# Kernel optimization log

Measured on AMD Instinct MI355X. Metric: run time of the kernel, lower is better.

## Reference

```python
import jax, jax.numpy as jnp
import numpy as np
import math

BS, SEQ, DIM, H, LK = 4, 4096, 768, 12, 256
HD = DIM // H  # 64
WIN = SEQ // LK  # 16, AdaptiveAvgPool1d reduces to uniform windows since SEQ % LK == 0


def setup_inputs() -> dict:
    key = jax.random.key(0)
    ks = jax.random.split(key, 12)
    s = 1.0 / math.sqrt(DIM)
    return {
        "query": jax.random.normal(ks[0], (BS, SEQ, DIM), jnp.float32),
        "key": jax.random.normal(ks[1], (BS, SEQ, DIM), jnp.float32),
        "value": jax.random.normal(ks[2], (BS, SEQ, DIM), jnp.float32),
        "mask": jax.random.normal(ks[3], (BS, SEQ), jnp.float32),  # mask<0 -> padded
        "Wq": jax.random.normal(ks[4], (DIM, DIM), jnp.float32) * s,
        "bq": jnp.zeros((DIM,), jnp.float32),
        "Wk": jax.random.normal(ks[5], (DIM, DIM), jnp.float32) * s,
        "bk": jnp.zeros((DIM,), jnp.float32),
        "Wv": jax.random.normal(ks[6], (DIM, DIM), jnp.float32) * s,
        "bv": jnp.zeros((DIM,), jnp.float32),
        "Wo": jax.random.normal(ks[7], (DIM, DIM), jnp.float32) * s,
        "bo": jnp.zeros((DIM,), jnp.float32),
    }


def reference(query, key, value, mask, Wq, bq, Wk, bk, Wv, bv, Wo, bo):
    bs, q_len, _ = query.shape
    # projections (nn.Linear: x @ W.T + b)
    Q = query @ Wq.T + bq
    K = key @ Wk.T + bk
    V = value @ Wv.T + bv
    # mask-fill padded K/V rows with 0 (mask dim==2 path: bool_mask = mask < 0)
    keep = (mask >= 0)[:, :, None]  # [bs, seq, 1]
    K = jnp.where(keep, K, 0.0)
    V = jnp.where(keep, V, 0.0)
    # adaptive avg pool over sequence -> linformer_k=256 (uniform windows of 16)
    Kc = K.reshape(bs, LK, WIN, DIM).mean(axis=2)  # [bs, 256, dim]
    Vc = V.reshape(bs, LK, WIN, DIM).mean(axis=2)
    # split heads
    Qh = Q.reshape(bs, q_len, H, HD) / math.sqrt(HD)  # scale fused
    Kh = Kc.reshape(bs, LK, H, HD)
    Vh = Vc.reshape(bs, LK, H, HD)
    # low-rank attention: [bs, h, q_len, 256]
    scores = jnp.einsum("bqhd,bkhd->bhqk", Qh, Kh)
    weights = jax.nn.softmax(scores, axis=-1)
    context = jnp.einsum("bhqk,bkhd->bqhd", weights, Vh).reshape(bs, q_len, DIM)
    return context @ Wo.T + bo
```

## Files before the change

### kernel.cpp

```cpp
#include <hip/hip_runtime.h>

#define BS_   4
#define SEQ_  4096
#define DIM_  768
#define NH_   12
#define HD_   64
#define LK_   256

typedef __attribute__((ext_vector_type(8))) short          bf8;
typedef __attribute__((ext_vector_type(8))) unsigned short us8;
typedef __attribute__((ext_vector_type(4))) unsigned short us4;
typedef __attribute__((ext_vector_type(4))) float          f32x4;

typedef unsigned int u32g __attribute__((address_space(1)));
typedef unsigned int u32l __attribute__((address_space(3)));

#define LOG2E 1.44269504088896340736f

__device__ __forceinline__ unsigned short f2bf(float f) {
  unsigned u = __builtin_bit_cast(unsigned, f);
  u += 0x7fffu + ((u >> 16) & 1u);
  return (unsigned short)(u >> 16);
}

__device__ __forceinline__ us8 cvt8(const float* __restrict__ p) {
  const float4 a = *(const float4*)p;
  const float4 b = *(const float4*)(p + 4);
  us8 r;
  r[0] = f2bf(a.x); r[1] = f2bf(a.y); r[2] = f2bf(a.z); r[3] = f2bf(a.w);
  r[4] = f2bf(b.x); r[5] = f2bf(b.y); r[6] = f2bf(b.z); r[7] = f2bf(b.w);
  return r;
}

__global__ __launch_bounds__(256) void cvtbf_kernel(
    const float* __restrict__ query,
    const float* __restrict__ Wq, const float* __restrict__ Wk,
    const float* __restrict__ Wv, const float* __restrict__ Wo,
    unsigned short* __restrict__ Qbf, unsigned short* __restrict__ Wbf)
{
  const int i = blockIdx.x * 256 + threadIdx.x;
  const int QN8 = (BS_ * SEQ_ * DIM_) / 8;
  const int WN8 = (DIM_ * DIM_) / 8;
  if (i < QN8) { *(us8*)(Qbf + (size_t)i * 8) = cvt8(query + (size_t)i * 8); return; }
  int j = i - QN8;
  const float* src; unsigned short* dst;
  if      (j <     WN8) { src = Wq; dst = Wbf;                   }
  else if (j < 2 * WN8) { src = Wk; dst = Wbf + DIM_*DIM_;     j -=     WN8; }
  else if (j < 3 * WN8) { src = Wv; dst = Wbf + 2*DIM_*DIM_;   j -= 2 * WN8; }
  else if (j < 4 * WN8) { src = Wo; dst = Wbf + 3*DIM_*DIM_;   j -= 3 * WN8; }
  else return;
  *(us8*)(dst + (size_t)j * 8) = cvt8(src + (size_t)j * 8);
}

__global__ __launch_bounds__(384) void pool_kernel(
    const float* __restrict__ key, const float* __restrict__ value,
    const float* __restrict__ mask,
    unsigned short* __restrict__ pk, unsigned short* __restrict__ pv,
    float* __restrict__ frac)
{
  const int blk = blockIdx.x;
  const int b = blk >> 8;
  const int l = blk & 255;
  const int tid = threadIdx.x;
  __shared__ float keep[16];
  if (tid < 16) keep[tid] = (mask[b * SEQ_ + l * 16 + tid] >= 0.f) ? 1.f : 0.f;
  __syncthreads();
  const int isV = tid >= 192;
  const int c = isV ? tid - 192 : tid;
  const float* src = isV ? value : key;
  float4 acc = make_float4(0.f, 0.f, 0.f, 0.f);
  #pragma unroll 1
  for (int w = 0; w < 16; ++w) {
    if (keep[w] != 0.f) {
      const float4 v = *(const float4*)(src + (size_t)(b * SEQ_ + l * 16 + w) * DIM_ + c * 4);
      acc.x += v.x; acc.y += v.y; acc.z += v.z; acc.w += v.w;
    }
  }
  const float s = 1.f / 16.f;
  unsigned short* dst = isV ? pv : pk;
  us4 o4;
  o4[0] = f2bf(acc.x * s); o4[1] = f2bf(acc.y * s);
  o4[2] = f2bf(acc.z * s); o4[3] = f2bf(acc.w * s);
  *(us4*)(dst + (size_t)(b * LK_ + l) * DIM_ + c * 4) = o4;
  if (tid == 0) {
    float cnt = 0.f;
    for (int w = 0; w < 16; ++w) cnt += keep[w];
    frac[b * LK_ + l] = cnt * s;
  }
}

template<int MODE, int SWZ>
__global__ __launch_bounds__(256) void gemm_bt(
    const void* __restrict__ Aptr_, const void* __restrict__ Bptr_,
    const float* __restrict__ bias, const float* __restrict__ bias2,
    const float* __restrict__ frac,
    void* __restrict__ Cout, float scale)
{
  constexpr int K = DIM_;
  __shared__ __align__(16) unsigned short lA[128 * 32];
  __shared__ __align__(16) unsigned short lB[128 * 32];
  const int tid  = threadIdx.x;
  const int lane = tid & 63;
  const int wave = tid >> 6;

  int bx, by;
  if (SWZ) {
    const int r = (blockIdx.x & 7) * 96 + (blockIdx.x >> 3);
    bx = r / 6; by = r % 6;
  } else {
    bx = blockIdx.x; by = blockIdx.y;
  }
  const int brow = bx * 128;
  const int bcol = by * 128;

  const unsigned short* A = (const unsigned short*)Aptr_;
  const unsigned short* Bw = (const unsigned short*)Bptr_;
  const float* bb = bias;
  int isV = 0;
  if (MODE == 34) {
    isV = blockIdx.z;
    A  += (size_t)isV * (BS_ * LK_ * DIM_);
    Bw += (size_t)isV * (DIM_ * DIM_);
    if (isV) bb = bias2;
  }

  const int wr   = (wave >> 1) * 64;
  const int wc   = (wave & 1) * 64;
  const int fr   = lane & 15;
  const int fk   = (lane >> 4) * 8;

  f32x4 acc[4][4];
  #pragma unroll
  for (int i = 0; i < 4; ++i)
    #pragma unroll
    for (int j = 0; j < 4; ++j) acc[i][j] = (f32x4){0.f, 0.f, 0.f, 0.f};

  const int srow = tid >> 2;
  const int schk = (tid & 3) * 8;

  for (int k0 = 0; k0 < K; k0 += 32) {
    __syncthreads();
    __builtin_amdgcn_global_load_lds(
        (const u32g*)(A + (size_t)(brow + srow) * K + k0 + schk),
        (u32l*)&lA[tid * 8], 16, 0, 0);
    __builtin_amdgcn_global_load_lds(
        (const u32g*)(A + (size_t)(brow + srow + 64) * K + k0 + schk),
        (u32l*)&lA[2048 + tid * 8], 16, 0, 0);
    __builtin_amdgcn_global_load_lds(
        (const u32g*)(Bw + (size_t)(bcol + srow) * K + k0 + schk),
        (u32l*)&lB[tid * 8], 16, 0, 0);
    __builtin_amdgcn_global_load_lds(
        (const u32g*)(Bw + (size_t)(bcol + srow + 64) * K + k0 + schk),
        (u32l*)&lB[2048 + tid * 8], 16, 0, 0);
    __syncthreads();
    bf8 af[4], bfv[4];
    #pragma unroll
    for (int mi = 0; mi < 4; ++mi)
      af[mi] = *(const bf8*)&lA[(wr + mi * 16 + fr) * 32 + fk];
    #pragma unroll
    for (int ni = 0; ni < 4; ++ni)
      bfv[ni] = *(const bf8*)&lB[(wc + ni * 16 + fr) * 32 + fk];
    #pragma unroll
    for (int mi = 0; mi < 4; ++mi)
      #pragma unroll
      for (int ni = 0; ni < 4; ++ni)
        acc[mi][ni] = __builtin_amdgcn_mfma_f32_16x16x32_bf16(af[mi], bfv[ni], acc[mi][ni], 0, 0, 0);
  }

  const int er = (lane >> 4) * 4;
  #pragma unroll
  for (int mi = 0; mi < 4; ++mi) {
    #pragma unroll
    for (int ni = 0; ni < 4; ++ni) {
      #pragma unroll
      for (int j = 0; j < 4; ++j) {
        const int r = brow + wr + mi * 16 + er + j;
        const int c = bcol + wc + ni * 16 + fr;
        float v = acc[mi][ni][j];
        if (MODE == 0) {
          v = (v + bias[c]) * scale;
          ((unsigned short*)Cout)[(size_t)r * DIM_ + c] = f2bf(v);
        } else if (MODE == 2) {
          ((float*)Cout)[(size_t)r * DIM_ + c] = v + bias[c];
        } else {
          v += frac[r] * bb[c];
          const int bb_ = r >> 8, key = r & 255;
          const int hh = c >> 6, dd = c & 63;
          const int bh = bb_ * NH_ + hh;
          size_t idx;
          if (isV) {
            idx = (size_t)bh * 16384 +
                ((key >> 5) * 4 + (dd >> 4)) * 512 + ((key >> 3) & 3) * 128 +
                (dd & 15) * 8 + (key & 7) + 786432;
          } else {
            const int t = key >> 5, g = (key >> 3) & 3, sub = (key >> 2) & 1, jj = key & 3;
            const int frk = g * 4 + jj;
            idx = (size_t)bh * 16384 +
                (((t * 2 + sub) * 2) + (dd >> 5)) * 512 + ((dd >> 3) & 3) * 128 +
                frk * 8 + (dd & 7);
          }
          ((unsigned short*)Cout)[idx] = f2bf(v);
        }
      }
    }
  }
}

__global__ __launch_bounds__(256) void attn_fused(
    const unsigned short* __restrict__ Qh,
    const unsigned short* __restrict__ Kf,
    const unsigned short* __restrict__ Vf,
    unsigned short* __restrict__ ctx)
{
  const int tid  = threadIdx.x;
  const int lane = tid & 63;
  const int wave = tid >> 6;
  const int bh = blockIdx.y;
  const int b = bh / NH_, h = bh % NH_;
  const int fr = lane & 15;
  const int hi = lane >> 4;
  const int qrow = blockIdx.x * 64 + wave * 16;

  const unsigned short* qp = Qh + (size_t)(b * SEQ_ + qrow + fr) * DIM_ + h * HD_ + hi * 8;
  const bf8 q0 = *(const bf8*)qp;
  const bf8 q1 = *(const bf8*)(qp + 32);

  const unsigned short* kb = Kf + (size_t)bh * 16384 + lane * 8;
  f32x4 scA[8], scB[8];
  __builtin_amdgcn_s_setprio(1);
  #pragma unroll
  for (int s = 0; s < 8; ++s) {
    const bf8 ka0 = *(const bf8*)(kb + (s * 4 + 0) * 512);
    const bf8 ka1 = *(const bf8*)(kb + (s * 4 + 1) * 512);
    const bf8 kb0 = *(const bf8*)(kb + (s * 4 + 2) * 512);
    const bf8 kb1 = *(const bf8*)(kb + (s * 4 + 3) * 512);
    f32x4 x = (f32x4){0.f, 0.f, 0.f, 0.f};
    x = __builtin_amdgcn_mfma_f32_16x16x32_bf16(ka0, q0, x, 0, 0, 0);
    x = __builtin_amdgcn_mfma_f32_16x16x32_bf16(ka1, q1, x, 0, 0, 0);
    scA[s] = x;
    f32x4 y = (f32x4){0.f, 0.f, 0.f, 0.f};
    y = __builtin_amdgcn_mfma_f32_16x16x32_bf16(kb0, q0, y, 0, 0, 0);
    y = __builtin_amdgcn_mfma_f32_16x16x32_bf16(kb1, q1, y, 0, 0, 0);
    scB[s] = y;
  }
  __builtin_amdgcn_s_setprio(0);

  float m = -1e30f;
  #pragma unroll
  for (int s = 0; s < 8; ++s)
    #pragma unroll
    for (int j = 0; j < 4; ++j) { m = fmaxf(m, scA[s][j]); m = fmaxf(m, scB[s][j]); }
  m = fmaxf(m, __shfl_xor(m, 16));
  m = fmaxf(m, __shfl_xor(m, 32));
  float sum = 0.f;
  #pragma unroll
  for (int s = 0; s < 8; ++s)
    #pragma unroll
    for (int j = 0; j < 4; ++j) {
      const float pa = exp2f(scA[s][j] - m); scA[s][j] = pa; sum += pa;
      const float pb = exp2f(scB[s][j] - m); scB[s][j] = pb; sum += pb;
    }
  sum += __shfl_xor(sum, 16);
  sum += __shfl_xor(sum, 32);
  const float inv = 1.f / sum;

  bf8 pa[8];
  #pragma unroll
  for (int s = 0; s < 8; ++s) {
    bf8 p;
    #pragma unroll
    for (int j = 0; j < 4; ++j) {
      p[j]     = (short)f2bf(scA[s][j] * inv);
      p[4 + j] = (short)f2bf(scB[s][j] * inv);
    }
    pa[s] = p;
  }

  const unsigned short* vb = Vf + (size_t)bh * 16384 + lane * 8;
  f32x4 acc[4];
  #pragma unroll
  for (int ct = 0; ct < 4; ++ct) acc[ct] = (f32x4){0.f, 0.f, 0.f, 0.f};
  __builtin_amdgcn_s_setprio(1);
  #pragma unroll
  for (int s = 0; s < 8; ++s) {
    #pragma unroll
    for (int ct = 0; ct < 4; ++ct) {
      const bf8 vf = *(const bf8*)(vb + (s * 4 + ct) * 512);
      acc[ct] = __builtin_amdgcn_mfma_f32_16x16x32_bf16(pa[s], vf, acc[ct], 0, 0, 0);
    }
  }
  __builtin_amdgcn_s_setprio(0);

  #pragma unroll
  for (int ct = 0; ct < 4; ++ct)
    #pragma unroll
    for (int j = 0; j < 4; ++j)
      ctx[(size_t)(b * SEQ_ + qrow + hi * 4 + j) * DIM_ + h * HD_ + ct * 16 + fr] =
          f2bf(acc[ct][j]);
}

extern "C" void kernel_launch(void* const* d_in, const int* in_sizes, int n_in,
                              void* d_out, int out_size, void* d_ws, size_t ws_size,
                              hipStream_t stream) {
  const float* query = (const float*)d_in[0];
  const float* key   = (const float*)d_in[1];
  const float* value = (const float*)d_in[2];
  const float* mask  = (const float*)d_in[3];
  const float* Wq    = (const float*)d_in[4];
  const float* bq    = (const float*)d_in[5];
  const float* Wk    = (const float*)d_in[6];
  const float* bk    = (const float*)d_in[7];
  const float* Wv    = (const float*)d_in[8];
  const float* bv    = (const float*)d_in[9];
  const float* Wo    = (const float*)d_in[10];
  const float* bo    = (const float*)d_in[11];
  float* out = (float*)d_out;

  char* ws = (char*)d_ws;
  unsigned short* Qh  = (unsigned short*)ws;
  unsigned short* ctx = (unsigned short*)(ws + 25165824);
  unsigned short* pK  = (unsigned short*)(ws + 50331648);
  unsigned short* pV  = (unsigned short*)(ws + 51904512);
  unsigned short* Kf  = (unsigned short*)(ws + 53477376);
  unsigned short* Vf  = (unsigned short*)(ws + 55050240);
  float*          frac = (float*)(ws + 56623104);
  unsigned short* Wbf = (unsigned short*)(ws + 56627200);
  unsigned short* Qbf = ctx;

  const float qscale = 0.125f * LOG2E;

  pool_kernel<<<dim3(1024), dim3(384), 0, stream>>>(key, value, mask, pK, pV, frac);
  cvtbf_kernel<<<dim3(7296), dim3(256), 0, stream>>>(query, Wq, Wk, Wv, Wo, Qbf, Wbf);
  gemm_bt<0, 1><<<dim3(768), dim3(256), 0, stream>>>(
      Qbf, Wbf, bq, nullptr, nullptr, Qh, qscale);
  gemm_bt<34, 0><<<dim3(8, 6, 2), dim3(256), 0, stream>>>(
      pK, Wbf + DIM_*DIM_, bk, bv, frac, Kf, 1.f);
  attn_fused<<<dim3(64, 48), dim3(256), 0, stream>>>(Qh, Kf, Vf, ctx);
  gemm_bt<2, 1><<<dim3(768), dim3(256), 0, stream>>>(
      ctx, Wbf + 3*DIM_*DIM_, bo, nullptr, nullptr, out, 1.f);
}
```

Measured before the change: 140.3 us.

## Fuse query fp32-to-bf16 conversion into Q GEMM and double attention rows per wave

Drops the separate pass that converts the query tensor to bf16. The Q projection GEMM now loads fp32 query tiles straight from global memory, converts them in registers and writes them to LDS, which saves writing and re-reading a 25MB intermediate. The attention kernel now has each wave process 32 query rows instead of 16, reusing every K/V fragment load for two MFMA chains, with half as many blocks and a launch-bounds occupancy hint. The GEMM A-side loses the async global-to-LDS load path and does synchronous register loads, and the attention kernel uses more registers.

```diff
diff --git a/kernel.cpp b/kernel.cpp
--- a/kernel.cpp
+++ b/kernel.cpp
@@ -33,16 +33,13 @@
 }
 
 __global__ __launch_bounds__(256) void cvtbf_kernel(
-    const float* __restrict__ query,
     const float* __restrict__ Wq, const float* __restrict__ Wk,
     const float* __restrict__ Wv, const float* __restrict__ Wo,
-    unsigned short* __restrict__ Qbf, unsigned short* __restrict__ Wbf)
+    unsigned short* __restrict__ Wbf)
 {
   const int i = blockIdx.x * 256 + threadIdx.x;
-  const int QN8 = (BS_ * SEQ_ * DIM_) / 8;
   const int WN8 = (DIM_ * DIM_) / 8;
-  if (i < QN8) { *(us8*)(Qbf + (size_t)i * 8) = cvt8(query + (size_t)i * 8); return; }
-  int j = i - QN8;
+  int j = i;
   const float* src; unsigned short* dst;
   if      (j <     WN8) { src = Wq; dst = Wbf;                   }
   else if (j < 2 * WN8) { src = Wk; dst = Wbf + DIM_*DIM_;     j -=     WN8; }
@@ -89,7 +86,7 @@
   }
 }
 
-template<int MODE, int SWZ>
+template<int SA, int MODE, int SWZ>
 __global__ __launch_bounds__(256) void gemm_bt(
     const void* __restrict__ Aptr_, const void* __restrict__ Bptr_,
     const float* __restrict__ bias, const float* __restrict__ bias2,
@@ -114,6 +111,7 @@
   const int bcol = by * 128;
 
   const unsigned short* A = (const unsigned short*)Aptr_;
+  const float*          Af = (const float*)Aptr_;
   const unsigned short* Bw = (const unsigned short*)Bptr_;
   const float* bb = bias;
   int isV = 0;
@@ -139,13 +137,23 @@
   const int schk = (tid & 3) * 8;
 
   for (int k0 = 0; k0 < K; k0 += 32) {
+    us8 a0, a1;
+    if (SA == 1) {
+      a0 = cvt8(Af + (size_t)(brow + srow) * K + k0 + schk);
+      a1 = cvt8(Af + (size_t)(brow + srow + 64) * K + k0 + schk);
+    }
     __syncthreads();
-    __builtin_amdgcn_global_load_lds(
-        (const u32g*)(A + (size_t)(brow + srow) * K + k0 + schk),
-        (u32l*)&lA[tid * 8], 16, 0, 0);
-    __builtin_amdgcn_global_load_lds(
-        (const u32g*)(A + (size_t)(brow + srow + 64) * K + k0 + schk),
-        (u32l*)&lA[2048 + tid * 8], 16, 0, 0);
+    if (SA == 0) {
+      __builtin_amdgcn_global_load_lds(
+          (const u32g*)(A + (size_t)(brow + srow) * K + k0 + schk),
+          (u32l*)&lA[tid * 8], 16, 0, 0);
+      __builtin_amdgcn_global_load_lds(
+          (const u32g*)(A + (size_t)(brow + srow + 64) * K + k0 + schk),
+          (u32l*)&lA[2048 + tid * 8], 16, 0, 0);
+    } else {
+      *(us8*)&lA[tid * 8]        = a0;
+      *(us8*)&lA[2048 + tid * 8] = a1;
+    }
     __builtin_amdgcn_global_load_lds(
         (const u32g*)(Bw + (size_t)(bcol + srow) * K + k0 + schk),
         (u32l*)&lB[tid * 8], 16, 0, 0);
@@ -206,7 +214,7 @@
   }
 }
 
-__global__ __launch_bounds__(256) void attn_fused(
+__global__ __launch_bounds__(256, 2) void attn_fused(
     const unsigned short* __restrict__ Qh,
     const unsigned short* __restrict__ Kf,
     const unsigned short* __restrict__ Vf,
@@ -219,14 +227,17 @@
   const int b = bh / NH_, h = bh % NH_;
   const int fr = lane & 15;
   const int hi = lane >> 4;
-  const int qrow = blockIdx.x * 64 + wave * 16;
-
-  const unsigned short* qp = Qh + (size_t)(b * SEQ_ + qrow + fr) * DIM_ + h * HD_ + hi * 8;
-  const bf8 q0 = *(const bf8*)qp;
-  const bf8 q1 = *(const bf8*)(qp + 32);
+  const int qrow0 = blockIdx.x * 128 + wave * 32;
+
+  const unsigned short* qp0 = Qh + (size_t)(b * SEQ_ + qrow0 + fr) * DIM_ + h * HD_ + hi * 8;
+  const unsigned short* qp1 = qp0 + 16 * DIM_;
+  const bf8 q00 = *(const bf8*)qp0;
+  const bf8 q01 = *(const bf8*)(qp0 + 32);
+  const bf8 q10 = *(const bf8*)qp1;
+  const bf8 q11 = *(const bf8*)(qp1 + 32);
 
   const unsigned short* kb = Kf + (size_t)bh * 16384 + lane * 8;
-  f32x4 scA[8], scB[8];
+  f32x4 sA0[8], sB0[8], sA1[8], sB1[8];
   __builtin_amdgcn_s_setprio(1);
   #pragma unroll
   for (int s = 0; s < 8; ++s) {
@@ -234,59 +245,84 @@
     const bf8 ka1 = *(const bf8*)(kb + (s * 4 + 1) * 512);
     const bf8 kb0 = *(const bf8*)(kb + (s * 4 + 2) * 512);
     const bf8 kb1 = *(const bf8*)(kb + (s * 4 + 3) * 512);
-    f32x4 x = (f32x4){0.f, 0.f, 0.f, 0.f};
-    x = __builtin_amdgcn_mfma_f32_16x16x32_bf16(ka0, q0, x, 0, 0, 0);
-    x = __builtin_amdgcn_mfma_f32_16x16x32_bf16(ka1, q1, x, 0, 0, 0);
-    scA[s] = x;
-    f32x4 y = (f32x4){0.f, 0.f, 0.f, 0.f};
-    y = __builtin_amdgcn_mfma_f32_16x16x32_bf16(kb0, q0, y, 0, 0, 0);
-    y = __builtin_amdgcn_mfma_f32_16x16x32_bf16(kb1, q1, y, 0, 0, 0);
-    scB[s] = y;
+    f32x4 x0 = (f32x4){0.f, 0.f, 0.f, 0.f};
+    x0 = __builtin_amdgcn_mfma_f32_16x16x32_bf16(ka0, q00, x0, 0, 0, 0);
+    x0 = __builtin_amdgcn_mfma_f32_16x16x32_bf16(ka1, q01, x0, 0, 0, 0);
+    sA0[s] = x0;
+    f32x4 y0 = (f32x4){0.f, 0.f, 0.f, 0.f};
+    y0 = __builtin_amdgcn_mfma_f32_16x16x32_bf16(kb0, q00, y0, 0, 0, 0);
+    y0 = __builtin_amdgcn_mfma_f32_16x16x32_bf16(kb1, q01, y0, 0, 0, 0);
+    sB0[s] = y0;
+    f32x4 x1 = (f32x4){0.f, 0.f, 0.f, 0.f};
+    x1 = __builtin_amdgcn_mfma_f32_16x16x32_bf16(ka0, q10, x1, 0, 0, 0);
+    x1 = __builtin_amdgcn_mfma_f32_16x16x32_bf16(ka1, q11, x1, 0, 0, 0);
+    sA1[s] = x1;
+    f32x4 y1 = (f32x4){0.f, 0.f, 0.f, 0.f};
+    y1 = __builtin_amdgcn_mfma_f32_16x16x32_bf16(kb0, q10, y1, 0, 0, 0);
+    y1 = __builtin_amdgcn_mfma_f32_16x16x32_bf16(kb1, q11, y1, 0, 0, 0);
+    sB1[s] = y1;
   }
   __builtin_amdgcn_s_setprio(0);
 
-  float m = -1e30f;
+  float m0 = -1e30f, m1 = -1e30f;
   #pragma unroll
   for (int s = 0; s < 8; ++s)
     #pragma unroll
-    for (int j = 0; j < 4; ++j) { m = fmaxf(m, scA[s][j]); m = fmaxf(m, scB[s][j]); }
-  m = fmaxf(m, __shfl_xor(m, 16));
-  m = fmaxf(m, __shfl_xor(m, 32));
-  float sum = 0.f;
+    for (int j = 0; j < 4; ++j) {
+      m0 = fmaxf(m0, sA0[s][j]); m0 = fmaxf(m0, sB0[s][j]);
+      m1 = fmaxf(m1, sA1[s][j]); m1 = fmaxf(m1, sB1[s][j]);
+    }
+  m0 = fmaxf(m0, __shfl_xor(m0, 16));
+  m0 = fmaxf(m0, __shfl_xor(m0, 32));
+  m1 = fmaxf(m1, __shfl_xor(m1, 16));
+  m1 = fmaxf(m1, __shfl_xor(m1, 32));
+  float u0 = 0.f, u1 = 0.f;
   #pragma unroll
   for (int s = 0; s < 8; ++s)
     #pragma unroll
     for (int j = 0; j < 4; ++j) {
-      const float pa = exp2f(scA[s][j] - m); scA[s][j] = pa; sum += pa;
-      const float pb = exp2f(scB[s][j] - m); scB[s][j] = pb; sum += pb;
-    }
-  sum += __shfl_xor(sum, 16);
-  sum += __shfl_xor(sum, 32);
-  const float inv = 1.f / sum;
-
-  bf8 pa[8];
+      float p;
+      p = exp2f(sA0[s][j] - m0); sA0[s][j] = p; u0 += p;
+      p = exp2f(sB0[s][j] - m0); sB0[s][j] = p; u0 += p;
+      p = exp2f(sA1[s][j] - m1); sA1[s][j] = p; u1 += p;
+      p = exp2f(sB1[s][j] - m1); sB1[s][j] = p; u1 += p;
+    }
+  u0 += __shfl_xor(u0, 16);
+  u0 += __shfl_xor(u0, 32);
+  u1 += __shfl_xor(u1, 16);
+  u1 += __shfl_xor(u1, 32);
+  const float inv0 = 1.f / u0;
+  const float inv1 = 1.f / u1;
+
+  bf8 pa0[8], pa1[8];
   #pragma unroll
   for (int s = 0; s < 8; ++s) {
-    bf8 p;
+    bf8 p0, p1;
     #pragma unroll
     for (int j = 0; j < 4; ++j) {
-      p[j]     = (short)f2bf(scA[s][j] * inv);
-      p[4 + j] = (short)f2bf(scB[s][j] * inv);
-    }
-    pa[s] = p;
+      p0[j]     = (short)f2bf(sA0[s][j] * inv0);
+      p0[4 + j] = (short)f2bf(sB0[s][j] * inv0);
+      p1[j]     = (short)f2bf(sA1[s][j] * inv1);
+      p1[4 + j] = (short)f2bf(sB1[s][j] * inv1);
+    }
+    pa0[s] = p0; pa1[s] = p1;
   }
 
   const unsigned short* vb = Vf + (size_t)bh * 16384 + lane * 8;
-  f32x4 acc[4];
-  #pragma unroll
-  for (int ct = 0; ct < 4; ++ct) acc[ct] = (f32x4){0.f, 0.f, 0.f, 0.f};
+  f32x4 acc0[4], acc1[4];
+  #pragma unroll
+  for (int ct = 0; ct < 4; ++ct) {
+    acc0[ct] = (f32x4){0.f, 0.f, 0.f, 0.f};
+    acc1[ct] = (f32x4){0.f, 0.f, 0.f, 0.f};
+  }
   __builtin_amdgcn_s_setprio(1);
   #pragma unroll
   for (int s = 0; s < 8; ++s) {
     #pragma unroll
     for (int ct = 0; ct < 4; ++ct) {
       const bf8 vf = *(const bf8*)(vb + (s * 4 + ct) * 512);
-      acc[ct] = __builtin_amdgcn_mfma_f32_16x16x32_bf16(pa[s], vf, acc[ct], 0, 0, 0);
+      acc0[ct] = __builtin_amdgcn_mfma_f32_16x16x32_bf16(pa0[s], vf, acc0[ct], 0, 0, 0);
+      acc1[ct] = __builtin_amdgcn_mfma_f32_16x16x32_bf16(pa1[s], vf, acc1[ct], 0, 0, 0);
     }
   }
   __builtin_amdgcn_s_setprio(0);
@@ -294,9 +330,12 @@
   #pragma unroll
   for (int ct = 0; ct < 4; ++ct)
     #pragma unroll
-    for (int j = 0; j < 4; ++j)
-      ctx[(size_t)(b * SEQ_ + qrow + hi * 4 + j) * DIM_ + h * HD_ + ct * 16 + fr] =
-          f2bf(acc[ct][j]);
+    for (int j = 0; j < 4; ++j) {
+      ctx[(size_t)(b * SEQ_ + qrow0 + hi * 4 + j) * DIM_ + h * HD_ + ct * 16 + fr] =
+          f2bf(acc0[ct][j]);
+      ctx[(size_t)(b * SEQ_ + qrow0 + 16 + hi * 4 + j) * DIM_ + h * HD_ + ct * 16 + fr] =
+          f2bf(acc1[ct][j]);
+    }
 }
 
 extern "C" void kernel_launch(void* const* d_in, const int* in_sizes, int n_in,
@@ -325,17 +364,16 @@
   unsigned short* Vf  = (unsigned short*)(ws + 55050240);
   float*          frac = (float*)(ws + 56623104);
   unsigned short* Wbf = (unsigned short*)(ws + 56627200);
-  unsigned short* Qbf = ctx;
 
   const float qscale = 0.125f * LOG2E;
 
   pool_kernel<<<dim3(1024), dim3(384), 0, stream>>>(key, value, mask, pK, pV, frac);
-  cvtbf_kernel<<<dim3(7296), dim3(256), 0, stream>>>(query, Wq, Wk, Wv, Wo, Qbf, Wbf);
-  gemm_bt<0, 1><<<dim3(768), dim3(256), 0, stream>>>(
-      Qbf, Wbf, bq, nullptr, nullptr, Qh, qscale);
-  gemm_bt<34, 0><<<dim3(8, 6, 2), dim3(256), 0, stream>>>(
+  cvtbf_kernel<<<dim3(1152), dim3(256), 0, stream>>>(Wq, Wk, Wv, Wo, Wbf);
+  gemm_bt<1, 0, 1><<<dim3(768), dim3(256), 0, stream>>>(
+      query, Wbf, bq, nullptr, nullptr, Qh, qscale);
+  gemm_bt<0, 34, 0><<<dim3(8, 6, 2), dim3(256), 0, stream>>>(
       pK, Wbf + DIM_*DIM_, bk, bv, frac, Kf, 1.f);
-  attn_fused<<<dim3(64, 48), dim3(256), 0, stream>>>(Qh, Kf, Vf, ctx);
-  gemm_bt<2, 1><<<dim3(768), dim3(256), 0, stream>>>(
+  attn_fused<<<dim3(32, 48), dim3(256), 0, stream>>>(Qh, Kf, Vf, ctx);
+  gemm_bt<0, 2, 1><<<dim3(768), dim3(256), 0, stream>>>(
       ctx, Wbf + 3*DIM_*DIM_, bo, nullptr, nullptr, out, 1.f);
 }
```

After: 152.1 us. +8.4%, slower.

## Fuse fp32 query conversion into Q GEMM and merge Q/KV projections into one launch

Applied to the files above, without the earlier changes.

The separate pass that converted the fp32 query to bf16 in a scratch buffer is removed. The Q projection GEMM now loads fp32 query rows into registers, converts them and stores them to LDS, and it shares one launch with the K/V projection blocks, with blocks indexed past 768 handling K/V. The softmax max and sum reductions in attention are restructured into vectorized tree reductions. This avoids a 50MB-scale write and read of the bf16 query copy plus one launch, but the Q path loses the async global-to-LDS load and now stalls on register loads before each LDS store.

```diff
diff --git a/kernel.cpp b/kernel.cpp
--- a/kernel.cpp
+++ b/kernel.cpp
@@ -32,17 +32,21 @@
   return r;
 }
 
+__device__ __forceinline__ f32x4 max4(f32x4 a, f32x4 b) {
+  f32x4 r;
+  r[0] = fmaxf(a[0], b[0]); r[1] = fmaxf(a[1], b[1]);
+  r[2] = fmaxf(a[2], b[2]); r[3] = fmaxf(a[3], b[3]);
+  return r;
+}
+
 __global__ __launch_bounds__(256) void cvtbf_kernel(
-    const float* __restrict__ query,
     const float* __restrict__ Wq, const float* __restrict__ Wk,
     const float* __restrict__ Wv, const float* __restrict__ Wo,
-    unsigned short* __restrict__ Qbf, unsigned short* __restrict__ Wbf)
+    unsigned short* __restrict__ Wbf)
 {
   const int i = blockIdx.x * 256 + threadIdx.x;
-  const int QN8 = (BS_ * SEQ_ * DIM_) / 8;
   const int WN8 = (DIM_ * DIM_) / 8;
-  if (i < QN8) { *(us8*)(Qbf + (size_t)i * 8) = cvt8(query + (size_t)i * 8); return; }
-  int j = i - QN8;
+  int j = i;
   const float* src; unsigned short* dst;
   if      (j <     WN8) { src = Wq; dst = Wbf;                   }
   else if (j < 2 * WN8) { src = Wk; dst = Wbf + DIM_*DIM_;     j -=     WN8; }
@@ -89,12 +93,13 @@
   }
 }
 
-template<int MODE, int SWZ>
-__global__ __launch_bounds__(256) void gemm_bt(
-    const void* __restrict__ Aptr_, const void* __restrict__ Bptr_,
-    const float* __restrict__ bias, const float* __restrict__ bias2,
-    const float* __restrict__ frac,
-    void* __restrict__ Cout, float scale)
+__global__ __launch_bounds__(256) void gemm_qkv(
+    const float* __restrict__ query, const unsigned short* __restrict__ Wbf,
+    const float* __restrict__ bq, const float* __restrict__ bk,
+    const float* __restrict__ bv, const float* __restrict__ frac,
+    const unsigned short* __restrict__ pKV,
+    unsigned short* __restrict__ Qh, unsigned short* __restrict__ KVf,
+    float qscale)
 {
   constexpr int K = DIM_;
   __shared__ __align__(16) unsigned short lA[128 * 32];
@@ -102,32 +107,31 @@
   const int tid  = threadIdx.x;
   const int lane = tid & 63;
   const int wave = tid >> 6;
-
-  int bx, by;
-  if (SWZ) {
-    const int r = (blockIdx.x & 7) * 96 + (blockIdx.x >> 3);
+  const int bid  = blockIdx.x;
+  const int isQ  = bid < 768;
+
+  int bx, by, isV = 0;
+  const unsigned short* Abf = nullptr;
+  const unsigned short* Bw;
+  if (isQ) {
+    const int r = (bid & 7) * 96 + (bid >> 3);
     bx = r / 6; by = r % 6;
+    Bw = Wbf;
   } else {
-    bx = blockIdx.x; by = blockIdx.y;
+    int kid = bid - 768;
+    isV = kid >= 48;
+    kid -= isV * 48;
+    bx = kid / 6; by = kid % 6;
+    Abf = pKV + (size_t)isV * (BS_ * LK_ * DIM_);
+    Bw  = Wbf + (size_t)(1 + isV) * (DIM_ * DIM_);
   }
   const int brow = bx * 128;
   const int bcol = by * 128;
 
-  const unsigned short* A = (const unsigned short*)Aptr_;
-  const unsigned short* Bw = (const unsigned short*)Bptr_;
-  const float* bb = bias;
-  int isV = 0;
-  if (MODE == 34) {
-    isV = blockIdx.z;
-    A  += (size_t)isV * (BS_ * LK_ * DIM_);
-    Bw += (size_t)isV * (DIM_ * DIM_);
-    if (isV) bb = bias2;
-  }
-
-  const int wr   = (wave >> 1) * 64;
-  const int wc   = (wave & 1) * 64;
-  const int fr   = lane & 15;
-  const int fk   = (lane >> 4) * 8;
+  const int wr = (wave >> 1) * 64;
+  const int wc = (wave & 1) * 64;
+  const int fr = lane & 15;
+  const int fk = (lane >> 4) * 8;
 
   f32x4 acc[4][4];
   #pragma unroll
@@ -139,13 +143,23 @@
   const int schk = (tid & 3) * 8;
 
   for (int k0 = 0; k0 < K; k0 += 32) {
+    us8 a0, a1;
+    if (isQ) {
+      a0 = cvt8(query + (size_t)(brow + srow) * K + k0 + schk);
+      a1 = cvt8(query + (size_t)(brow + srow + 64) * K + k0 + schk);
+    }
     __syncthreads();
-    __builtin_amdgcn_global_load_lds(
-        (const u32g*)(A + (size_t)(brow + srow) * K + k0 + schk),
-        (u32l*)&lA[tid * 8], 16, 0, 0);
-    __builtin_amdgcn_global_load_lds(
-        (const u32g*)(A + (size_t)(brow + srow + 64) * K + k0 + schk),
-        (u32l*)&lA[2048 + tid * 8], 16, 0, 0);
+    if (isQ) {
+      *(us8*)&lA[tid * 8]        = a0;
+      *(us8*)&lA[2048 + tid * 8] = a1;
+    } else {
+      __builtin_amdgcn_global_load_lds(
+          (const u32g*)(Abf + (size_t)(brow + srow) * K + k0 + schk),
+          (u32l*)&lA[tid * 8], 16, 0, 0);
+      __builtin_amdgcn_global_load_lds(
+          (const u32g*)(Abf + (size_t)(brow + srow + 64) * K + k0 + schk),
+          (u32l*)&lA[2048 + tid * 8], 16, 0, 0);
+    }
     __builtin_amdgcn_global_load_lds(
         (const u32g*)(Bw + (size_t)(bcol + srow) * K + k0 + schk),
         (u32l*)&lB[tid * 8], 16, 0, 0);
@@ -177,13 +191,11 @@
         const int r = brow + wr + mi * 16 + er + j;
         const int c = bcol + wc + ni * 16 + fr;
         float v = acc[mi][ni][j];
-        if (MODE == 0) {
-          v = (v + bias[c]) * scale;
-          ((unsigned short*)Cout)[(size_t)r * DIM_ + c] = f2bf(v);
-        } else if (MODE == 2) {
-          ((float*)Cout)[(size_t)r * DIM_ + c] = v + bias[c];
+        if (isQ) {
+          v = (v + bq[c]) * qscale;
+          Qh[(size_t)r * DIM_ + c] = f2bf(v);
         } else {
-          v += frac[r] * bb[c];
+          v += frac[r] * (isV ? bv[c] : bk[c]);
           const int bb_ = r >> 8, key = r & 255;
           const int hh = c >> 6, dd = c & 63;
           const int bh = bb_ * NH_ + hh;
@@ -199,11 +211,80 @@
                 (((t * 2 + sub) * 2) + (dd >> 5)) * 512 + ((dd >> 3) & 3) * 128 +
                 frk * 8 + (dd & 7);
           }
-          ((unsigned short*)Cout)[idx] = f2bf(v);
+          KVf[idx] = f2bf(v);
         }
       }
     }
   }
+}
+
+__global__ __launch_bounds__(256) void gemm_out(
+    const unsigned short* __restrict__ A, const unsigned short* __restrict__ Bw,
+    const float* __restrict__ bias, float* __restrict__ Cout)
+{
+  constexpr int K = DIM_;
+  __shared__ __align__(16) unsigned short lA[128 * 32];
+  __shared__ __align__(16) unsigned short lB[128 * 32];
+  const int tid  = threadIdx.x;
+  const int lane = tid & 63;
+  const int wave = tid >> 6;
+  const int r0 = (blockIdx.x & 7) * 96 + (blockIdx.x >> 3);
+  const int brow = (r0 / 6) * 128;
+  const int bcol = (r0 % 6) * 128;
+  const int wr = (wave >> 1) * 64;
+  const int wc = (wave & 1) * 64;
+  const int fr = lane & 15;
+  const int fk = (lane >> 4) * 8;
+
+  f32x4 acc[4][4];
+  #pragma unroll
+  for (int i = 0; i < 4; ++i)
+    #pragma unroll
+    for (int j = 0; j < 4; ++j) acc[i][j] = (f32x4){0.f, 0.f, 0.f, 0.f};
+
+  const int srow = tid >> 2;
+  const int schk = (tid & 3) * 8;
+
+  for (int k0 = 0; k0 < K; k0 += 32) {
+    __syncthreads();
+    __builtin_amdgcn_global_load_lds(
+        (const u32g*)(A + (size_t)(brow + srow) * K + k0 + schk),
+        (u32l*)&lA[tid * 8], 16, 0, 0);
+    __builtin_amdgcn_global_load_lds(
+        (const u32g*)(A + (size_t)(brow + srow + 64) * K + k0 + schk),
+        (u32l*)&lA[2048 + tid * 8], 16, 0, 0);
+    __builtin_amdgcn_global_load_lds(
+        (const u32g*)(Bw + (size_t)(bcol + srow) * K + k0 + schk),
+        (u32l*)&lB[tid * 8], 16, 0, 0);
+    __builtin_amdgcn_global_load_lds(
+        (const u32g*)(Bw + (size_t)(bcol + srow + 64) * K + k0 + schk),
+        (u32l*)&lB[2048 + tid * 8], 16, 0, 0);
+    __syncthreads();
+    bf8 af[4], bfv[4];
+    #pragma unroll
+    for (int mi = 0; mi < 4; ++mi)
+      af[mi] = *(const bf8*)&lA[(wr + mi * 16 + fr) * 32 + fk];
+    #pragma unroll
+    for (int ni = 0; ni < 4; ++ni)
+      bfv[ni] = *(const bf8*)&lB[(wc + ni * 16 + fr) * 32 + fk];
+    #pragma unroll
+    for (int mi = 0; mi < 4; ++mi)
+      #pragma unroll
+      for (int ni = 0; ni < 4; ++ni)
+        acc[mi][ni] = __builtin_amdgcn_mfma_f32_16x16x32_bf16(af[mi], bfv[ni], acc[mi][ni], 0, 0, 0);
+  }
+
+  const int er = (lane >> 4) * 4;
+  #pragma unroll
+  for (int mi = 0; mi < 4; ++mi)
+    #pragma unroll
+    for (int ni = 0; ni < 4; ++ni)
+      #pragma unroll
+      for (int j = 0; j < 4; ++j) {
+        const int r = brow + wr + mi * 16 + er + j;
+        const int c = bcol + wc + ni * 16 + fr;
+        Cout[(size_t)r * DIM_ + c] = acc[mi][ni][j] + bias[c];
+      }
 }
 
 __global__ __launch_bounds__(256) void attn_fused(
@@ -245,21 +326,31 @@
   }
   __builtin_amdgcn_s_setprio(0);
 
-  float m = -1e30f;
-  #pragma unroll
-  for (int s = 0; s < 8; ++s)
-    #pragma unroll
-    for (int j = 0; j < 4; ++j) { m = fmaxf(m, scA[s][j]); m = fmaxf(m, scB[s][j]); }
+  f32x4 tm[8];
+  #pragma unroll
+  for (int s = 0; s < 8; ++s) tm[s] = max4(scA[s], scB[s]);
+  tm[0] = max4(tm[0], tm[4]); tm[1] = max4(tm[1], tm[5]);
+  tm[2] = max4(tm[2], tm[6]); tm[3] = max4(tm[3], tm[7]);
+  tm[0] = max4(tm[0], tm[2]); tm[1] = max4(tm[1], tm[3]);
+  tm[0] = max4(tm[0], tm[1]);
+  float m = fmaxf(fmaxf(tm[0][0], tm[0][1]), fmaxf(tm[0][2], tm[0][3]));
   m = fmaxf(m, __shfl_xor(m, 16));
   m = fmaxf(m, __shfl_xor(m, 32));
-  float sum = 0.f;
-  #pragma unroll
-  for (int s = 0; s < 8; ++s)
+
+  f32x4 uA = (f32x4){0.f, 0.f, 0.f, 0.f};
+  f32x4 uB = (f32x4){0.f, 0.f, 0.f, 0.f};
+  #pragma unroll
+  for (int s = 0; s < 8; ++s) {
     #pragma unroll
     for (int j = 0; j < 4; ++j) {
-      const float pa = exp2f(scA[s][j] - m); scA[s][j] = pa; sum += pa;
-      const float pb = exp2f(scB[s][j] - m); scB[s][j] = pb; sum += pb;
-    }
+      scA[s][j] = exp2f(scA[s][j] - m);
+      scB[s][j] = exp2f(scB[s][j] - m);
+    }
+    uA += scA[s];
+    uB += scB[s];
+  }
+  const f32x4 uv = uA + uB;
+  float sum = (uv[0] + uv[1]) + (uv[2] + uv[3]);
   sum += __shfl_xor(sum, 16);
   sum += __shfl_xor(sum, 32);
   const float inv = 1.f / sum;
@@ -325,17 +416,13 @@
   unsigned short* Vf  = (unsigned short*)(ws + 55050240);
   float*          frac = (float*)(ws + 56623104);
   unsigned short* Wbf = (unsigned short*)(ws + 56627200);
-  unsigned short* Qbf = ctx;
 
   const float qscale = 0.125f * LOG2E;
 
   pool_kernel<<<dim3(1024), dim3(384), 0, stream>>>(key, value, mask, pK, pV, frac);
-  cvtbf_kernel<<<dim3(7296), dim3(256), 0, stream>>>(query, Wq, Wk, Wv, Wo, Qbf, Wbf);
-  gemm_bt<0, 1><<<dim3(768), dim3(256), 0, stream>>>(
-      Qbf, Wbf, bq, nullptr, nullptr, Qh, qscale);
-  gemm_bt<34, 0><<<dim3(8, 6, 2), dim3(256), 0, stream>>>(
-      pK, Wbf + DIM_*DIM_, bk, bv, frac, Kf, 1.f);
+  cvtbf_kernel<<<dim3(1152), dim3(256), 0, stream>>>(Wq, Wk, Wv, Wo, Wbf);
+  gemm_qkv<<<dim3(864), dim3(256), 0, stream>>>(
+      query, Wbf, bq, bk, bv, frac, pK, Qh, Kf, qscale);
   attn_fused<<<dim3(64, 48), dim3(256), 0, stream>>>(Qh, Kf, Vf, ctx);
-  gemm_bt<2, 1><<<dim3(768), dim3(256), 0, stream>>>(
-      ctx, Wbf + 3*DIM_*DIM_, bo, nullptr, nullptr, out, 1.f);
-}
+  gemm_out<<<dim3(768), dim3(256), 0, stream>>>(ctx, Wbf + 3*DIM_*DIM_, bo, out);
+}
```

Result: slower. 149.0 us (+6.2%).
